# Optimization experiments

Measured on AMD Instinct MI355X. Metric: run time of the kernel, lower is better.

The kernel has to match this reference:

```python
import jax, jax.numpy as jnp
import numpy as np


def setup_inputs() -> dict:
    key = jax.random.key(0)
    k1, k2 = jax.random.split(key)
    B, t, nbands, framesize = 32, 4000, 65, 80
    H = jax.random.normal(k1, (B, t, nbands), dtype=jnp.float32)
    noise = jax.random.uniform(k2, (B, t, framesize), dtype=jnp.float32)  # uniform [0,1); scaled to [-1,1) in reference
    return {"H": H, "noise": noise, "framesize": framesize}


def reference(H, noise, framesize):
    # H: [B, t, nbands] real half-spectrum of zero-phase filter
    B, t, nbands = H.shape
    L_fir = 2 * nbands - 1  # FIR length (129)

    # zero-phase impulse response -> linear-phase via circular shift
    zero_phase = jnp.fft.irfft(H, n=L_fir, axis=-1)          # [B, t, L_fir]
    lin_phase = jnp.roll(zero_phase, nbands - 1, axis=-1)

    # periodic Hann window (matches torch.hann_window default periodic=True)
    n = jnp.arange(L_fir, dtype=H.dtype)
    hann = 0.5 * (1.0 - jnp.cos(2.0 * jnp.pi * n / L_fir))
    firwin = lin_phase * hann                                 # [B, t, L_fir]

    # per-frame noise in [-1, 1)
    x = noise * 2.0 - 1.0                                     # [B, t, framesize]

    # full FFT convolution along last axis
    L = framesize + L_fir - 1                                 # 208
    X = jnp.fft.rfft(x, n=L, axis=-1)
    W = jnp.fft.rfft(firwin, n=L, axis=-1)
    filtered = jnp.fft.irfft(X * W, n=L, axis=-1)             # [B, t, L]

    # overlap-add with hop = framesize via scatter-add (replaces conv_transpose1d trick)
    total = (t - 1) * framesize + L
    idx = jnp.arange(t)[:, None] * framesize + jnp.arange(L)[None, :]  # [t, L]
    out = jnp.zeros((B, total), dtype=filtered.dtype).at[:, idx].add(filtered)

    # trim filter group delay from both ends -> [B, t*framesize]
    return out[:, nbands - 1: total - (nbands - 1)]
```

## Files before the change

kernel.cpp:

```cpp
#include <hip/hip_runtime.h>


#define NT 256
#define X_STRIDE 84
#define XPAD 8
#define W_STRIDE 154
#define W_P 24
#define NSLOT 35
#define WTOT_H 5416
#define XTOT_H 2948

typedef _Float16 f16x8 __attribute__((ext_vector_type(8)));
typedef _Float16 f16x4 __attribute__((ext_vector_type(4)));
typedef _Float16 h2 __attribute__((ext_vector_type(2)));
typedef float f32x4 __attribute__((ext_vector_type(4)));

union U32H2 { unsigned u; h2 h; };
static __device__ __forceinline__ h2 mid_h2(h2 lo, h2 hi) {
  U32H2 a, b; a.h = lo; b.h = hi;
  U32H2 o; o.u = __builtin_amdgcn_alignbit(b.u, a.u, 16);
  return o.h;
}

__global__ void __launch_bounds__(256)
minit_kernel(_Float16* __restrict__ M) {
  const float TP = 6.28318530717958647692f / 129.f;
  int i = blockIdx.x * 256 + threadIdx.x;
  int frag = i >> 9;
  int off  = i & 511;
  int lane = off >> 3, j = off & 7;
  int nt = frag / 3, ks = frag - 3 * (frag / 3);
  int n = nt * 16 + (lane & 15);
  int k = ks * 32 + (lane >> 4) * 8 + j;
  float v = 0.f;
  if (n <= 128 && k <= 64) {
    float hann = 0.5f - 0.5f * __cosf((float)n * TP);
    float sc = (k == 0 ? 1.f : 2.f) * (1.f / 129.f);
    int e = (k * (n - 64)) % 129; if (e < 0) e += 129;
    v = hann * sc * __cosf((float)e * TP);
  }
  M[i] = (_Float16)v;
}

__global__ void __launch_bounds__(NT, 8)
fng_kernel(const float* __restrict__ Hg_, const float* __restrict__ Ng_,
           float* __restrict__ Og_, const _Float16* __restrict__ Mg) {
  __shared__ __align__(16) _Float16 sWh[WTOT_H];
  __shared__ __align__(16) _Float16 sXh[XTOT_H];

  const int t  = threadIdx.x;
  const int bx = blockIdx.x;
  const int b  = blockIdx.y;
  const int f0 = bx * 32;

  const int wv   = t >> 6;
  const int lane = t & 63;

  float c0[8], c1[8];
  float s64 = 0.f;
  bool  va  = false;
  {
    if (wv < 3) {
      const int quad = lane >> 4;
      const int l15  = lane & 15;
      const int fr   = f0 - 2 + wv * 16 + l15;
      va = (fr >= 0 && fr < 4000);
      const int frc  = va ? fr : 0;
      const float* hr = Hg_ + (size_t)b * 260000 + (size_t)frc * 65;
      __builtin_memcpy(c0, &hr[quad * 8], 32);
      __builtin_memcpy(c1, &hr[32 + quad * 8], 32);
      s64 = hr[64];
    }
  }

  {
#pragma unroll
    for (int it = 0; it < 4; ++it) {
      int j = t + NT * it;
      if (j < 24) {
        sWh[j] = (_Float16)0.f;
      } else if (j < 899) {
        int jj = j - 24;
        int c = jj / 25, o = jj - 25 * c;
        sWh[c * W_STRIDE + 153 + o] = (_Float16)0.f;
      }
    }
  }

  {
    const float* Ng = Ng_ + (size_t)b * 320000;
#pragma unroll
    for (int j = 0; j < 3; ++j) {
      int q = t + NT * j;
      if (q < NSLOT * 20) {
        int fi = q / 20, qm = q - 20 * fi;
        int fr = f0 - 2 + fi;
        f16x4 o = {(_Float16)0.f, (_Float16)0.f, (_Float16)0.f, (_Float16)0.f};
        if (fr >= 0 && fr < 4000) {
          float4 v = *(const float4*)&Ng[(size_t)fr * 80 + 4 * qm];
          o.x = (_Float16)(2.f * v.w - 1.f);
          o.y = (_Float16)(2.f * v.z - 1.f);
          o.z = (_Float16)(2.f * v.y - 1.f);
          o.w = (_Float16)(2.f * v.x - 1.f);
        }
        *(f16x4*)&sXh[XPAD + fi * X_STRIDE + (76 - 4 * qm)] = o;
      }
    }
  }

  {
    if (wv < 3) {
      const int quad = lane >> 4;
      const int l15  = lane & 15;
      const int mt   = wv;
      if (!va) {
#pragma unroll
        for (int j = 0; j < 8; ++j) { c0[j] = 0.f; c1[j] = 0.f; }
        s64 = 0.f;
      }
      f16x8 a0, a1, a2;
#pragma unroll
      for (int j = 0; j < 8; ++j) {
        a0[j] = (_Float16)c0[j];
        a1[j] = (_Float16)c1[j];
        a2[j] = (_Float16)0.f;
      }
      if (quad == 0) a2[0] = (_Float16)s64;

#pragma unroll 3
      for (int nt = 0; nt < 9; ++nt) {
        f32x4 acc = {0.f, 0.f, 0.f, 0.f};
        f16x8 b0 = ((const f16x8*)Mg)[(nt * 3 + 0) * 64 + lane];
        f16x8 b1 = ((const f16x8*)Mg)[(nt * 3 + 1) * 64 + lane];
        f16x8 b2 = ((const f16x8*)Mg)[(nt * 3 + 2) * 64 + lane];
        acc = __builtin_amdgcn_mfma_f32_16x16x32_f16(a0, b0, acc, 0, 0, 0);
        acc = __builtin_amdgcn_mfma_f32_16x16x32_f16(a1, b1, acc, 0, 0, 0);
        acc = __builtin_amdgcn_mfma_f32_16x16x32_f16(a2, b2, acc, 0, 0, 0);
        const int n = nt * 16 + l15;
        if (n <= 128) {
          const int fb = mt * 16 + quad * 4;
#pragma unroll
          for (int r = 0; r < 4; ++r) {
            int frame = fb + r;
            if (frame < NSLOT) sWh[frame * W_STRIDE + W_P + n] = (_Float16)acc[r];
          }
        }
      }
    }
  }
  __syncthreads();

  {
    const int col = t & 31;
    const int pb  = t >> 5;
    const int e   = 64 + 10 * pb;
    const int qq  = (e >= 80) ? 1 : 0;
    const int D   = e - 80 * qq;
    float acc[10];
#pragma unroll
    for (int i = 0; i < 10; ++i) acc[i] = 0.f;

#pragma unroll 1
    for (int g = 2; g >= -1; --g) {
      const int dlt = D + 80 * g;
      int Ulo = (dlt - 128) >> 3; if (Ulo < 0) Ulo = 0;
      int Uhi = (dlt + 9) >> 3;   if (Uhi > 9) Uhi = 9;
      if (Ulo > Uhi) continue;
      const int slot = col + qq - g + 2;
      const _Float16* wr = &sWh[slot * W_STRIDE];
      const _Float16* xr = &sXh[XPAD + slot * X_STRIDE];
      int wb = W_P + dlt - 8 * Ulo - 4;

      h2 wEa[10], wOa[9];
#pragma unroll
      for (int k2 = 0; k2 < 10; ++k2) wEa[k2] = *(const h2*)&wr[wb - 4 + 2 * k2];
#pragma unroll
      for (int k2 = 0; k2 < 9; ++k2) wOa[k2] = mid_h2(wEa[k2], wEa[k2 + 1]);

      const _Float16* xp = &xr[72 - 8 * Ulo];
      f16x4 p0 = *(const f16x4*)&xp[0];
      f16x4 p1 = *(const f16x4*)&xp[4];

#define PAIRX(K) (((K) & 1) ? wOa[(((K) - 1) >> 1) + 2] : wEa[(((K) >> 1) + 2)])
#pragma unroll 4
      for (int U = Ulo; U <= Uhi; ++U) {
        f16x4 q0 = p0, q1 = p1;
        xp -= 8;
        p0 = *(const f16x4*)&xp[0];
        p1 = *(const f16x4*)&xp[4];
        h2 xD; xD.x = q0.x; xD.y = q0.y;
        h2 xC; xC.x = q0.z; xC.y = q0.w;
        h2 xB; xB.x = q1.x; xB.y = q1.y;
        h2 xA; xA.x = q1.z; xA.y = q1.w;
#pragma unroll
        for (int i = 0; i < 10; ++i) {
          float a = acc[i];
          a = __builtin_amdgcn_fdot2(xA, PAIRX(i + 3), a, false);
          a = __builtin_amdgcn_fdot2(xB, PAIRX(i + 1), a, false);
          a = __builtin_amdgcn_fdot2(xC, PAIRX(i - 1), a, false);
          a = __builtin_amdgcn_fdot2(xD, PAIRX(i - 3), a, false);
          acc[i] = a;
        }
        const _Float16* wp = &wr[wb - 12];
#pragma unroll
        for (int k2 = 9; k2 >= 4; --k2) wEa[k2] = wEa[k2 - 4];
#pragma unroll
        for (int k2 = 8; k2 >= 4; --k2) wOa[k2] = wOa[k2 - 4];
        wEa[0] = *(const h2*)&wp[0];
        wEa[1] = *(const h2*)&wp[2];
        wEa[2] = *(const h2*)&wp[4];
        wEa[3] = *(const h2*)&wp[6];
        wOa[0] = mid_h2(wEa[0], wEa[1]);
        wOa[1] = mid_h2(wEa[1], wEa[2]);
        wOa[2] = mid_h2(wEa[2], wEa[3]);
        wOa[3] = mid_h2(wEa[3], wEa[4]);
        wb -= 8;
      }
#undef PAIRX
    }

    float* Ob = Og_ + (size_t)b * 320000 + 2560 * bx + 80 * col + 10 * pb;
#pragma unroll
    for (int s = 0; s < 5; ++s) {
      float2 v; v.x = acc[2 * s]; v.y = acc[2 * s + 1];
      *(float2*)&Ob[2 * s] = v;
    }
  }
}

extern "C" void kernel_launch(void* const* d_in, const int* in_sizes, int n_in,
                              void* d_out, int out_size, void* d_ws, size_t ws_size,
                              hipStream_t stream) {
  const float* H     = (const float*)d_in[0];
  const float* noise = (const float*)d_in[1];
  float* out = (float*)d_out;
  _Float16* M = (_Float16*)d_ws;
  (void)in_sizes; (void)n_in; (void)ws_size; (void)out_size;

  minit_kernel<<<54, 256, 0, stream>>>(M);
  dim3 grid(125, 32, 1);
  fng_kernel<<<grid, NT, 0, stream>>>(H, noise, out, M);
}
```

Measured before the change: 151.5 us.

## Replace fp16 fdot2 overlap-add inner loop with packed fp32 FMA using register rotation

```diff
diff --git a/kernel.cpp b/kernel.cpp
--- a/kernel.cpp
+++ b/kernel.cpp
@@ -14,12 +14,10 @@
 typedef _Float16 f16x4 __attribute__((ext_vector_type(4)));
 typedef _Float16 h2 __attribute__((ext_vector_type(2)));
 typedef float f32x4 __attribute__((ext_vector_type(4)));
-
-union U32H2 { unsigned u; h2 h; };
-static __device__ __forceinline__ h2 mid_h2(h2 lo, h2 hi) {
-  U32H2 a, b; a.h = lo; b.h = hi;
-  U32H2 o; o.u = __builtin_amdgcn_alignbit(b.u, a.u, 16);
-  return o.h;
+typedef float f32x2 __attribute__((ext_vector_type(2)));
+
+static __device__ __forceinline__ f32x2 cv2(h2 h) {
+  f32x2 r; r.x = (float)h.x; r.y = (float)h.y; return r;
 }
 
 __global__ void __launch_bounds__(256)
@@ -42,7 +40,7 @@
   M[i] = (_Float16)v;
 }
 
-__global__ void __launch_bounds__(NT, 8)
+__global__ void __launch_bounds__(NT, 7)
 fng_kernel(const float* __restrict__ Hg_, const float* __restrict__ Ng_,
            float* __restrict__ Og_, const _Float16* __restrict__ Mg) {
   __shared__ __align__(16) _Float16 sWh[WTOT_H];
@@ -156,9 +154,45 @@
     const int e   = 64 + 10 * pb;
     const int qq  = (e >= 80) ? 1 : 0;
     const int D   = e - 80 * qq;
-    float acc[10];
-#pragma unroll
-    for (int i = 0; i < 10; ++i) acc[i] = 0.f;
+    f32x2 PA0 = {0.f, 0.f}, PA1 = {0.f, 0.f}, PA2 = {0.f, 0.f},
+          PA3 = {0.f, 0.f}, PA4 = {0.f, 0.f};
+    f32x2 PB0 = {0.f, 0.f}, PB1 = {0.f, 0.f}, PB2 = {0.f, 0.f},
+          PB3 = {0.f, 0.f}, PB4 = {0.f, 0.f}, PB5 = {0.f, 0.f};
+
+#define PK(P, X, W) P = __builtin_elementwise_fma(X, W, P)
+#define TRIP(W0,W1,W2,W3,W4,W5,W6,W7,W8, F0,F1,F2,F3, QC0,QC1, QN0,QN1)      \
+  { h2 t0_ = *(const h2*)&wq[-8]; h2 t1_ = *(const h2*)&wq[-6];               \
+    h2 t2_ = *(const h2*)&wq[-4]; h2 t3_ = *(const h2*)&wq[-2];               \
+    xp -= 8;                                                                  \
+    QN0 = *(const f16x4*)&xp[0];                                              \
+    QN1 = *(const f16x4*)&xp[4];                                              \
+    float xs0 = (float)QC1.w, xs1 = (float)QC1.z;                             \
+    float xs2 = (float)QC1.y, xs3 = (float)QC1.x;                             \
+    float xs4 = (float)QC0.w, xs5 = (float)QC0.z;                             \
+    float xs6 = (float)QC0.y, xs7 = (float)QC0.x;                             \
+    f32x2 X;                                                                  \
+    X.x = xs0; X.y = xs0;                                                     \
+    PK(PA0,X,W4); PK(PA1,X,W5); PK(PA2,X,W6); PK(PA3,X,W7); PK(PA4,X,W8);     \
+    X.x = xs1; X.y = xs1;                                                     \
+    PK(PB0,X,W3); PK(PB1,X,W4); PK(PB2,X,W5); PK(PB3,X,W6); PK(PB4,X,W7);     \
+    PK(PB5,X,W8);                                                             \
+    X.x = xs2; X.y = xs2;                                                     \
+    PK(PA0,X,W3); PK(PA1,X,W4); PK(PA2,X,W5); PK(PA3,X,W6); PK(PA4,X,W7);     \
+    X.x = xs3; X.y = xs3;                                                     \
+    PK(PB0,X,W2); PK(PB1,X,W3); PK(PB2,X,W4); PK(PB3,X,W5); PK(PB4,X,W6);     \
+    PK(PB5,X,W7);                                                             \
+    X.x = xs4; X.y = xs4;                                                     \
+    PK(PA0,X,W2); PK(PA1,X,W3); PK(PA2,X,W4); PK(PA3,X,W5); PK(PA4,X,W6);     \
+    X.x = xs5; X.y = xs5;                                                     \
+    PK(PB0,X,W1); PK(PB1,X,W2); PK(PB2,X,W3); PK(PB3,X,W4); PK(PB4,X,W5);     \
+    PK(PB5,X,W6);                                                             \
+    X.x = xs6; X.y = xs6;                                                     \
+    PK(PA0,X,W1); PK(PA1,X,W2); PK(PA2,X,W3); PK(PA3,X,W4); PK(PA4,X,W5);     \
+    X.x = xs7; X.y = xs7;                                                     \
+    PK(PB0,X,W0); PK(PB1,X,W1); PK(PB2,X,W2); PK(PB3,X,W3); PK(PB4,X,W4);     \
+    PK(PB5,X,W5);                                                             \
+    F0 = cv2(t0_); F1 = cv2(t1_); F2 = cv2(t2_); F3 = cv2(t3_);               \
+    wq -= 8; }
 
 #pragma unroll 1
     for (int g = 2; g >= -1; --g) {
@@ -169,62 +203,49 @@
       const int slot = col + qq - g + 2;
       const _Float16* wr = &sWh[slot * W_STRIDE];
       const _Float16* xr = &sXh[XPAD + slot * X_STRIDE];
-      int wb = W_P + dlt - 8 * Ulo - 4;
-
-      h2 wEa[10], wOa[9];
-#pragma unroll
-      for (int k2 = 0; k2 < 10; ++k2) wEa[k2] = *(const h2*)&wr[wb - 4 + 2 * k2];
-#pragma unroll
-      for (int k2 = 0; k2 < 9; ++k2) wOa[k2] = mid_h2(wEa[k2], wEa[k2 + 1]);
-
+
+      const _Float16* wq = wr + (16 + dlt - 8 * Ulo);
+      f32x2 R0 = cv2(*(const h2*)&wq[0]);
+      f32x2 R1 = cv2(*(const h2*)&wq[2]);
+      f32x2 R2 = cv2(*(const h2*)&wq[4]);
+      f32x2 R3 = cv2(*(const h2*)&wq[6]);
+      f32x2 R4 = cv2(*(const h2*)&wq[8]);
+      f32x2 R5 = cv2(*(const h2*)&wq[10]);
+      f32x2 R6 = cv2(*(const h2*)&wq[12]);
+      f32x2 R7 = cv2(*(const h2*)&wq[14]);
+      f32x2 R8 = cv2(*(const h2*)&wq[16]);
+      f32x2 R9, R10, R11, R12, R13, R14, R15;
       const _Float16* xp = &xr[72 - 8 * Ulo];
-      f16x4 p0 = *(const f16x4*)&xp[0];
-      f16x4 p1 = *(const f16x4*)&xp[4];
-
-#define PAIRX(K) (((K) & 1) ? wOa[(((K) - 1) >> 1) + 2] : wEa[(((K) >> 1) + 2)])
-#pragma unroll 4
-      for (int U = Ulo; U <= Uhi; ++U) {
-        f16x4 q0 = p0, q1 = p1;
-        xp -= 8;
-        p0 = *(const f16x4*)&xp[0];
-        p1 = *(const f16x4*)&xp[4];
-        h2 xD; xD.x = q0.x; xD.y = q0.y;
-        h2 xC; xC.x = q0.z; xC.y = q0.w;
-        h2 xB; xB.x = q1.x; xB.y = q1.y;
-        h2 xA; xA.x = q1.z; xA.y = q1.w;
-#pragma unroll
-        for (int i = 0; i < 10; ++i) {
-          float a = acc[i];
-          a = __builtin_amdgcn_fdot2(xA, PAIRX(i + 3), a, false);
-          a = __builtin_amdgcn_fdot2(xB, PAIRX(i + 1), a, false);
-          a = __builtin_amdgcn_fdot2(xC, PAIRX(i - 1), a, false);
-          a = __builtin_amdgcn_fdot2(xD, PAIRX(i - 3), a, false);
-          acc[i] = a;
-        }
-        const _Float16* wp = &wr[wb - 12];
-#pragma unroll
-        for (int k2 = 9; k2 >= 4; --k2) wEa[k2] = wEa[k2 - 4];
-#pragma unroll
-        for (int k2 = 8; k2 >= 4; --k2) wOa[k2] = wOa[k2 - 4];
-        wEa[0] = *(const h2*)&wp[0];
-        wEa[1] = *(const h2*)&wp[2];
-        wEa[2] = *(const h2*)&wp[4];
-        wEa[3] = *(const h2*)&wp[6];
-        wOa[0] = mid_h2(wEa[0], wEa[1]);
-        wOa[1] = mid_h2(wEa[1], wEa[2]);
-        wOa[2] = mid_h2(wEa[2], wEa[3]);
-        wOa[3] = mid_h2(wEa[3], wEa[4]);
-        wb -= 8;
-      }
-#undef PAIRX
-    }
-
+      f16x4 qa0 = *(const f16x4*)&xp[0];
+      f16x4 qa1 = *(const f16x4*)&xp[4];
+      f16x4 qb0, qb1;
+
+      int U = Ulo;
+      for (;;) {
+        TRIP(R0,R1,R2,R3,R4,R5,R6,R7,R8,    R12,R13,R14,R15, qa0,qa1, qb0,qb1)
+        if (++U > Uhi) break;
+        TRIP(R12,R13,R14,R15,R0,R1,R2,R3,R4, R8,R9,R10,R11,  qb0,qb1, qa0,qa1)
+        if (++U > Uhi) break;
+        TRIP(R8,R9,R10,R11,R12,R13,R14,R15,R0, R4,R5,R6,R7,  qa0,qa1, qb0,qb1)
+        if (++U > Uhi) break;
+        TRIP(R4,R5,R6,R7,R8,R9,R10,R11,R12,  R0,R1,R2,R3,    qb0,qb1, qa0,qa1)
+        if (++U > Uhi) break;
+      }
+    }
+#undef TRIP
+#undef PK
+
+    float o0 = PA0.x + PB0.y, o1 = PA0.y + PB1.x;
+    float o2 = PA1.x + PB1.y, o3 = PA1.y + PB2.x;
+    float o4 = PA2.x + PB2.y, o5 = PA2.y + PB3.x;
+    float o6 = PA3.x + PB3.y, o7 = PA3.y + PB4.x;
+    float o8 = PA4.x + PB4.y, o9 = PA4.y + PB5.x;
     float* Ob = Og_ + (size_t)b * 320000 + 2560 * bx + 80 * col + 10 * pb;
-#pragma unroll
-    for (int s = 0; s < 5; ++s) {
-      float2 v; v.x = acc[2 * s]; v.y = acc[2 * s + 1];
-      *(float2*)&Ob[2 * s] = v;
-    }
+    float2 v0; v0.x = o0; v0.y = o1; *(float2*)&Ob[0] = v0;
+    float2 v1; v1.x = o2; v1.y = o3; *(float2*)&Ob[2] = v1;
+    float2 v2; v2.x = o4; v2.y = o5; *(float2*)&Ob[4] = v2;
+    float2 v3; v3.x = o6; v3.y = o7; *(float2*)&Ob[6] = v3;
+    float2 v4; v4.x = o8; v4.y = o9; *(float2*)&Ob[8] = v4;
   }
 }
 
```

Measured after the change: 157.8 us. 1.04x slower.
